# Performance work log

Measured on AMD Instinct MI355X. Metric: run time of the kernel, lower is better.

The kernel has to match this reference:

```python
import jax, jax.numpy as jnp
import numpy as np

N_NODES = 50000
N_EDGES = 400000


def setup_inputs() -> dict:
    key = jax.random.key(0)
    ks = jax.random.split(key, 8)
    d_in, d_hid, d_out = 512, 512, 256
    feats = jax.random.normal(ks[0], (N_NODES, d_in), dtype=jnp.float32)
    src = jax.random.randint(ks[1], (N_EDGES,), 0, N_NODES, dtype=jnp.int32)
    dst = jax.random.randint(ks[2], (N_EDGES,), 0, N_NODES, dtype=jnp.int32)
    # Glorot-ish scaled weights so activations stay O(1)
    W0 = jax.random.normal(ks[3], (d_in, d_hid), dtype=jnp.float32) / np.sqrt(d_in)
    b0 = jnp.zeros((d_hid,), jnp.float32)
    W1 = jax.random.normal(ks[4], (d_hid, d_hid), dtype=jnp.float32) / np.sqrt(d_hid)
    b1 = jnp.zeros((d_hid,), jnp.float32)
    W2 = jax.random.normal(ks[5], (d_hid, d_out), dtype=jnp.float32) / np.sqrt(d_hid)
    b2 = jnp.zeros((d_out,), jnp.float32)
    return {"feats": feats, "src": src, "dst": dst,
            "W0": W0, "b0": b0, "W1": W1, "b1": b1, "W2": W2, "b2": b2}


def _sage_conv_gcn(h, src, dst, W, b, deg):
    # DGL SAGEConv aggregator_type='gcn':
    # h_neigh[v] = (sum_{u->v} h[u] + h[v]) / (in_deg(v) + 1); out = h_neigh @ W + b
    agg = jax.ops.segment_sum(h[src], dst, num_segments=h.shape[0])  # [N, d]
    h_neigh = (agg + h) / (deg[:, None] + 1.0)
    return h_neigh @ W + b


def reference(feats, src, dst, W0, b0, W1, b1, W2, b2):
    N = feats.shape[0]
    deg = jax.ops.segment_sum(jnp.ones((src.shape[0],), feats.dtype), dst,
                              num_segments=N)  # in-degree per node
    h = jax.nn.relu(_sage_conv_gcn(feats, src, dst, W0, b0, deg))  # dropout p=0, norm none
    h = jax.nn.relu(_sage_conv_gcn(h, src, dst, W1, b1, deg))
    h = _sage_conv_gcn(h, src, dst, W2, b2, deg)  # final layer: no activation
    return h
```

## Files before the change

### kernel.cpp

```cpp
#include <hip/hip_runtime.h>
#include <stdint.h>

#define N_NODES 50000
#define N_EDGES 400000
#define MPAD    50048
#define SCAN_B  49

typedef __bf16 bf16x8 __attribute__((ext_vector_type(8)));
typedef float  f32x4  __attribute__((ext_vector_type(4)));
typedef unsigned short ushort_t;
typedef unsigned int   uint_t;

__device__ __forceinline__ ushort_t f2b(float f){
    uint_t x = __float_as_uint(f);
    x += 0x7FFFu + ((x >> 16) & 1u);
    return (ushort_t)(x >> 16);
}
__device__ __forceinline__ float b2f(ushort_t h){
    return __uint_as_float(((uint_t)h) << 16);
}

__global__ void zero_two(int* a, int* b, int n){
    int i = blockIdx.x * blockDim.x + threadIdx.x;
    if (i < n){ a[i] = 0; b[i] = 0; }
}

__global__ void hist_kernel(const int* __restrict__ dst, int* __restrict__ deg, int E){
    int i = blockIdx.x * blockDim.x + threadIdx.x;
    if (i < E) atomicAdd(&deg[dst[i]], 1);
}

__global__ __launch_bounds__(1024) void blk_scan_kernel(
        const int* __restrict__ deg, int* __restrict__ offs,
        int* __restrict__ bsum, int n){
    __shared__ int buf[1024];
    const int t = threadIdx.x, b = blockIdx.x;
    const int i = b * 1024 + t;
    int v = (i < n) ? deg[i] : 0;
    buf[t] = v; __syncthreads();
    for (int off = 1; off < 1024; off <<= 1){
        int x = (t >= off) ? buf[t - off] : 0;
        __syncthreads();
        buf[t] += x;
        __syncthreads();
    }
    if (i < n) offs[i] = buf[t] - v;
    if (t == 1023) bsum[b] = buf[1023];
}

__global__ void bsum_scan_kernel(int* __restrict__ bsum, int nb){
    int t = threadIdx.x;
    int orig = (t < nb) ? bsum[t] : 0;
    int v = orig;
    #pragma unroll
    for (int off = 1; off < 64; off <<= 1){
        int x = __shfl_up(v, off, 64);
        if (t >= off) v += x;
    }
    if (t < nb) bsum[t] = v - orig;
}

__global__ __launch_bounds__(1024) void add_off_kernel(
        int* __restrict__ offs, const int* __restrict__ bsum, int n){
    int i = blockIdx.x * 1024 + threadIdx.x;
    if (i < n) offs[i] += bsum[blockIdx.x];
    if (i == 0) offs[n] = N_EDGES;
}

__global__ void fill_kernel(const int* __restrict__ src, const int* __restrict__ dst,
                            const int* __restrict__ offs, int* __restrict__ cursor,
                            int* __restrict__ nbr, int E){
    int i = blockIdx.x * blockDim.x + threadIdx.x;
    if (i < E){
        int d = dst[i];
        int p = atomicAdd(&cursor[d], 1);
        nbr[offs[d] + p] = src[i];
    }
}

__global__ void wtrans_kernel(const float* __restrict__ W, ushort_t* __restrict__ Wt,
                              int K, int N){
    int i = blockIdx.x * blockDim.x + threadIdx.x;
    if (i < K * N){
        int n = i / K, k = i - n * K;
        Wt[i] = f2b(W[k * N + n]);
    }
}

__device__ __forceinline__ void load16(const void* g, void* l){
    __builtin_amdgcn_global_load_lds((const __attribute__((address_space(1))) void*)g,
                                     (__attribute__((address_space(3))) void*)l, 16, 0, 0);
}

__global__ __launch_bounds__(256, 2) void gemm_bt512(const ushort_t* __restrict__ A,
                                                     const ushort_t* __restrict__ Bt,
                                                     ushort_t* __restrict__ C,
                                                     int K){
    __shared__ ushort_t As[64 * 32];
    __shared__ ushort_t Bs[512 * 32];
    const int tid  = threadIdx.x, lane = tid & 63, wave = tid >> 6;
    const int bm = blockIdx.x;
    const int fr = lane & 15;
    const int fk = (lane >> 4) * 8;
    const int wn = wave * 128;
    f32x4 acc[4][8] = {};

    for (int kt = 0; kt < K; kt += 32){
        __syncthreads();
        {
            int s = tid;
            load16(A + (size_t)(bm * 64 + (s >> 2)) * K + kt + (s & 3) * 8,
                   (char*)As + s * 16);
        }
        #pragma unroll
        for (int i = 0; i < 8; i++){
            int s = tid + i * 256;
            load16(Bt + (size_t)(s >> 2) * K + kt + (s & 3) * 8,
                   (char*)Bs + s * 16);
        }
        __syncthreads();
        bf16x8 af[4], bf[8];
        #pragma unroll
        for (int t = 0; t < 4; t++)
            af[t] = *(const bf16x8*)(const void*)(As + (t * 16 + fr) * 32 + fk);
        #pragma unroll
        for (int t = 0; t < 8; t++)
            bf[t] = *(const bf16x8*)(const void*)(Bs + (wn + t * 16 + fr) * 32 + fk);
        #pragma unroll
        for (int tm = 0; tm < 4; tm++)
            #pragma unroll
            for (int tn = 0; tn < 8; tn++)
                acc[tm][tn] = __builtin_amdgcn_mfma_f32_16x16x32_bf16(
                                  af[tm], bf[tn], acc[tm][tn], 0, 0, 0);
    }
    const int r0 = (lane >> 4) * 4, c0 = lane & 15;
    #pragma unroll
    for (int tm = 0; tm < 4; tm++){
        #pragma unroll
        for (int tn = 0; tn < 8; tn++){
            int rbase = bm * 64 + tm * 16 + r0;
            int cidx  = wn + tn * 16 + c0;
            #pragma unroll
            for (int reg = 0; reg < 4; reg++)
                C[(size_t)(rbase + reg) * 512 + cidx] = f2b(acc[tm][tn][reg]);
        }
    }
}

__global__ __launch_bounds__(256, 2) void gemm_a32(const float* __restrict__ A,
                                                   const ushort_t* __restrict__ Bt,
                                                   ushort_t* __restrict__ C,
                                                   int K){
    __shared__ ushort_t As[64 * 32];
    __shared__ ushort_t Bs[512 * 32];
    const int tid  = threadIdx.x, lane = tid & 63, wave = tid >> 6;
    const int bm = blockIdx.x;
    const int fr = lane & 15;
    const int fk = (lane >> 4) * 8;
    const int wn = wave * 128;
    f32x4 acc[4][8] = {};

    for (int kt = 0; kt < K; kt += 32){
        __syncthreads();
        #pragma unroll
        for (int i = 0; i < 8; i++){
            int s = tid + i * 256;
            load16(Bt + (size_t)(s >> 2) * K + kt + (s & 3) * 8,
                   (char*)Bs + s * 16);
        }
        {
            int s = tid;
            int row = bm * 64 + (s >> 2);
            uint4 o = make_uint4(0u, 0u, 0u, 0u);
            if (row < N_NODES){
                const float* p = A + (size_t)row * K + kt + (s & 3) * 8;
                float4 x = *(const float4*)(const void*)p;
                float4 y = *(const float4*)(const void*)(p + 4);
                o.x = (uint_t)f2b(x.x) | ((uint_t)f2b(x.y) << 16);
                o.y = (uint_t)f2b(x.z) | ((uint_t)f2b(x.w) << 16);
                o.z = (uint_t)f2b(y.x) | ((uint_t)f2b(y.y) << 16);
                o.w = (uint_t)f2b(y.z) | ((uint_t)f2b(y.w) << 16);
            }
            *(uint4*)(void*)((char*)As + s * 16) = o;
        }
        __syncthreads();
        bf16x8 af[4], bf[8];
        #pragma unroll
        for (int t = 0; t < 4; t++)
            af[t] = *(const bf16x8*)(const void*)(As + (t * 16 + fr) * 32 + fk);
        #pragma unroll
        for (int t = 0; t < 8; t++)
            bf[t] = *(const bf16x8*)(const void*)(Bs + (wn + t * 16 + fr) * 32 + fk);
        #pragma unroll
        for (int tm = 0; tm < 4; tm++)
            #pragma unroll
            for (int tn = 0; tn < 8; tn++)
                acc[tm][tn] = __builtin_amdgcn_mfma_f32_16x16x32_bf16(
                                  af[tm], bf[tn], acc[tm][tn], 0, 0, 0);
    }
    const int r0 = (lane >> 4) * 4, c0 = lane & 15;
    #pragma unroll
    for (int tm = 0; tm < 4; tm++){
        #pragma unroll
        for (int tn = 0; tn < 8; tn++){
            int rbase = bm * 64 + tm * 16 + r0;
            int cidx  = wn + tn * 16 + c0;
            #pragma unroll
            for (int reg = 0; reg < 4; reg++)
                C[(size_t)(rbase + reg) * 512 + cidx] = f2b(acc[tm][tn][reg]);
        }
    }
}

__global__ __launch_bounds__(256, 2) void gemm_bt(const ushort_t* __restrict__ A,
                                                  const ushort_t* __restrict__ Bt,
                                                  ushort_t* __restrict__ C,
                                                  int N, int K){
    __shared__ ushort_t As[128 * 32];
    __shared__ ushort_t Bs[256 * 32];
    const int tid  = threadIdx.x, lane = tid & 63, wave = tid >> 6;
    const int bm = blockIdx.x, bn = blockIdx.y;
    const int fr = lane & 15;
    const int fk = (lane >> 4) * 8;
    const int wm = (wave >> 1) * 64, wn = (wave & 1) * 128;
    f32x4 acc[4][8] = {};

    for (int kt = 0; kt < K; kt += 32){
        __syncthreads();
        #pragma unroll
        for (int i = 0; i < 2; i++){
            int s = tid + i * 256;
            load16(A + (size_t)(bm * 128 + (s >> 2)) * K + kt + (s & 3) * 8,
                   (char*)As + s * 16);
        }
        #pragma unroll
        for (int i = 0; i < 4; i++){
            int s = tid + i * 256;
            load16(Bt + (size_t)(bn * 256 + (s >> 2)) * K + kt + (s & 3) * 8,
                   (char*)Bs + s * 16);
        }
        __syncthreads();
        bf16x8 af[4], bf[8];
        #pragma unroll
        for (int t = 0; t < 4; t++)
            af[t] = *(const bf16x8*)(const void*)(As + (wm + t * 16 + fr) * 32 + fk);
        #pragma unroll
        for (int t = 0; t < 8; t++)
            bf[t] = *(const bf16x8*)(const void*)(Bs + (wn + t * 16 + fr) * 32 + fk);
        #pragma unroll
        for (int tm = 0; tm < 4; tm++)
            #pragma unroll
            for (int tn = 0; tn < 8; tn++)
                acc[tm][tn] = __builtin_amdgcn_mfma_f32_16x16x32_bf16(
                                  af[tm], bf[tn], acc[tm][tn], 0, 0, 0);
    }
    const int r0 = (lane >> 4) * 4, c0 = lane & 15;
    #pragma unroll
    for (int tm = 0; tm < 4; tm++){
        #pragma unroll
        for (int tn = 0; tn < 8; tn++){
            int rbase = bm * 128 + wm + tm * 16 + r0;
            int cidx  = bn * 256 + wn + tn * 16 + c0;
            #pragma unroll
            for (int reg = 0; reg < 4; reg++)
                C[(size_t)(rbase + reg) * N + cidx] = f2b(acc[tm][tn][reg]);
        }
    }
}

__device__ __forceinline__ void acc8(float* a, uint4 y){
    a[0] += b2f((ushort_t)(y.x & 0xffff)); a[1] += b2f((ushort_t)(y.x >> 16));
    a[2] += b2f((ushort_t)(y.y & 0xffff)); a[3] += b2f((ushort_t)(y.y >> 16));
    a[4] += b2f((ushort_t)(y.z & 0xffff)); a[5] += b2f((ushort_t)(y.z >> 16));
    a[6] += b2f((ushort_t)(y.w & 0xffff)); a[7] += b2f((ushort_t)(y.w >> 16));
}
__device__ __forceinline__ void acc4(float* a, uint2 y){
    a[0] += b2f((ushort_t)(y.x & 0xffff)); a[1] += b2f((ushort_t)(y.x >> 16));
    a[2] += b2f((ushort_t)(y.y & 0xffff)); a[3] += b2f((ushort_t)(y.y >> 16));
}

__global__ __launch_bounds__(512) void agg_relu_kernel(
        const ushort_t* __restrict__ Y, const int* __restrict__ offs,
        const int* __restrict__ nbr, const float* __restrict__ bias,
        ushort_t* __restrict__ H){
    const int lane = threadIdx.x & 63, wv = threadIdx.x >> 6;
    const int v   = blockIdx.x * 4 + (wv >> 1);
    const int off = (wv & 1) * 256 + lane * 4;
    float a[4];
    {   uint2 y = *(const uint2*)(const void*)(Y + (size_t)v * 512 + off);
        a[0] = b2f((ushort_t)(y.x & 0xffff)); a[1] = b2f((ushort_t)(y.x >> 16));
        a[2] = b2f((ushort_t)(y.y & 0xffff)); a[3] = b2f((ushort_t)(y.y >> 16)); }
    const int beg = offs[v], end = offs[v + 1];
    int i = beg;
    for (; i + 8 <= end; i += 8){
        uint2 yy[8];
        #pragma unroll
        for (int j = 0; j < 8; j++){
            int u = nbr[i + j];
            yy[j] = *(const uint2*)(const void*)(Y + (size_t)u * 512 + off);
        }
        #pragma unroll
        for (int j = 0; j < 8; j++) acc4(a, yy[j]);
    }
    for (; i + 4 <= end; i += 4){
        uint2 yy[4];
        #pragma unroll
        for (int j = 0; j < 4; j++){
            int u = nbr[i + j];
            yy[j] = *(const uint2*)(const void*)(Y + (size_t)u * 512 + off);
        }
        #pragma unroll
        for (int j = 0; j < 4; j++) acc4(a, yy[j]);
    }
    for (; i < end; i++){
        int u = nbr[i];
        uint2 y = *(const uint2*)(const void*)(Y + (size_t)u * 512 + off);
        acc4(a, y);
    }
    const float inv = 1.0f / (float)(end - beg + 1);
    float4 bb = ((const float4*)bias)[(wv & 1) * 64 + lane];
    float r[4];
    r[0] = a[0]*inv + bb.x; r[1] = a[1]*inv + bb.y;
    r[2] = a[2]*inv + bb.z; r[3] = a[3]*inv + bb.w;
    #pragma unroll
    for (int j = 0; j < 4; j++) r[j] = r[j] > 0.f ? r[j] : 0.f;
    uint2 o;
    o.x = (uint_t)f2b(r[0]) | ((uint_t)f2b(r[1]) << 16);
    o.y = (uint_t)f2b(r[2]) | ((uint_t)f2b(r[3]) << 16);
    *(uint2*)(void*)(H + (size_t)v * 512 + off) = o;
}

__global__ __launch_bounds__(256) void agg_out_kernel(
        const ushort_t* __restrict__ Y, const int* __restrict__ offs,
        const int* __restrict__ nbr, const float* __restrict__ bias,
        float* __restrict__ out){
    const int lane = threadIdx.x & 63, wave = threadIdx.x >> 6;
    const int v = blockIdx.x * 4 + wave;
    const int off = lane * 4;
    float a[4];
    {   uint2 y = *(const uint2*)(const void*)(Y + (size_t)v * 256 + off);
        a[0] = b2f((ushort_t)(y.x & 0xffff)); a[1] = b2f((ushort_t)(y.x >> 16));
        a[2] = b2f((ushort_t)(y.y & 0xffff)); a[3] = b2f((ushort_t)(y.y >> 16)); }
    const int beg = offs[v], end = offs[v + 1];
    int i = beg;
    for (; i + 8 <= end; i += 8){
        uint2 yy[8];
        #pragma unroll
        for (int j = 0; j < 8; j++){
            int u = nbr[i + j];
            yy[j] = *(const uint2*)(const void*)(Y + (size_t)u * 256 + off);
        }
        #pragma unroll
        for (int j = 0; j < 8; j++) acc4(a, yy[j]);
    }
    for (; i + 4 <= end; i += 4){
        uint2 yy[4];
        #pragma unroll
        for (int j = 0; j < 4; j++){
            int u = nbr[i + j];
            yy[j] = *(const uint2*)(const void*)(Y + (size_t)u * 256 + off);
        }
        #pragma unroll
        for (int j = 0; j < 4; j++) acc4(a, yy[j]);
    }
    for (; i < end; i++){
        int u = nbr[i];
        uint2 y = *(const uint2*)(const void*)(Y + (size_t)u * 256 + off);
        acc4(a, y);
    }
    const float inv = 1.0f / (float)(end - beg + 1);
    float4 bb = ((const float4*)bias)[lane];
    float4 r;
    r.x = a[0]*inv + bb.x; r.y = a[1]*inv + bb.y;
    r.z = a[2]*inv + bb.z; r.w = a[3]*inv + bb.w;
    ((float4*)out)[v * 64 + lane] = r;
}

extern "C" void kernel_launch(void* const* d_in, const int* in_sizes, int n_in,
                              void* d_out, int out_size, void* d_ws, size_t ws_size,
                              hipStream_t stream) {
    const float* feats = (const float*)d_in[0];
    const int*   src   = (const int*)  d_in[1];
    const int*   dst   = (const int*)  d_in[2];
    const float* W0    = (const float*)d_in[3];
    const float* b0    = (const float*)d_in[4];
    const float* W1    = (const float*)d_in[5];
    const float* b1    = (const float*)d_in[6];
    const float* W2    = (const float*)d_in[7];
    const float* b2    = (const float*)d_in[8];
    float* out = (float*)d_out;

    char* w = (char*)d_ws;
    ushort_t* Abuf = (ushort_t*)w;  w += (size_t)MPAD * 512 * 2;
    ushort_t* Ybuf = (ushort_t*)w;  w += (size_t)MPAD * 512 * 2;
    ushort_t* W0t  = (ushort_t*)w;  w += 512 * 512 * 2;
    ushort_t* W1t  = (ushort_t*)w;  w += 512 * 512 * 2;
    ushort_t* W2t  = (ushort_t*)w;  w += 256 * 512 * 2;
    int* deg    = (int*)w;          w += 50048 * 4;
    int* offs   = (int*)w;          w += 50056 * 4;
    int* cursor = (int*)w;          w += 50048 * 4;
    int* nbr    = (int*)w;          w += (size_t)N_EDGES * 4;
    int* bsum   = (int*)w;          w += 64 * 4;

    zero_two<<<(N_NODES + 255) / 256, 256, 0, stream>>>(deg, cursor, N_NODES);
    hist_kernel<<<(N_EDGES + 255) / 256, 256, 0, stream>>>(dst, deg, N_EDGES);
    blk_scan_kernel<<<SCAN_B, 1024, 0, stream>>>(deg, offs, bsum, N_NODES);
    bsum_scan_kernel<<<1, 64, 0, stream>>>(bsum, SCAN_B);
    add_off_kernel<<<SCAN_B, 1024, 0, stream>>>(offs, bsum, N_NODES);
    fill_kernel<<<(N_EDGES + 255) / 256, 256, 0, stream>>>(src, dst, offs, cursor, nbr, N_EDGES);

    wtrans_kernel<<<(512 * 512 + 255) / 256, 256, 0, stream>>>(W0, W0t, 512, 512);
    wtrans_kernel<<<(512 * 512 + 255) / 256, 256, 0, stream>>>(W1, W1t, 512, 512);
    wtrans_kernel<<<(512 * 256 + 255) / 256, 256, 0, stream>>>(W2, W2t, 512, 256);

    gemm_a32<<<MPAD / 64, 256, 0, stream>>>(feats, W0t, Ybuf, 512);
    agg_relu_kernel<<<N_NODES / 4, 512, 0, stream>>>(Ybuf, offs, nbr, b0, Abuf);
    gemm_bt512<<<MPAD / 64, 256, 0, stream>>>(Abuf, W1t, Ybuf, 512);
    agg_relu_kernel<<<N_NODES / 4, 512, 0, stream>>>(Ybuf, offs, nbr, b1, Abuf);
    dim3 g2(MPAD / 128, 1);
    gemm_bt<<<g2, 256, 0, stream>>>(Abuf, W2t, Ybuf, 256, 512);
    agg_out_kernel<<<N_NODES / 4, 256, 0, stream>>>(Ybuf, offs, nbr, b2, out);
}
```

Baseline: 519.1 us.

## Replace GEMMs with unified 128x128 tile kernel using XOR-swizzled LDS and K=64 steps

The three per-layer GEMM kernels are replaced by 128x128-tile kernels that use a 2D grid over rows and output columns. Each tile advances K in steps of 64 and stores data in LDS with an XOR swizzle to avoid bank conflicts on fragment reads. The fp32-input variant now issues all of its global loads before converting to bf16. Launch bounds allow more blocks per CU, which is meant to raise occupancy and reduce LDS conflicts, but each block now reloads A once per column tile.

```diff
diff --git a/kernel.cpp b/kernel.cpp
--- a/kernel.cpp
+++ b/kernel.cpp
@@ -92,119 +92,141 @@
                                      (__attribute__((address_space(3))) void*)l, 16, 0, 0);
 }
 
-__global__ __launch_bounds__(256, 2) void gemm_bt512(const ushort_t* __restrict__ A,
+__global__ __launch_bounds__(256, 4) void gemm128_bt(const ushort_t* __restrict__ A,
                                                      const ushort_t* __restrict__ Bt,
                                                      ushort_t* __restrict__ C,
-                                                     int K){
-    __shared__ ushort_t As[64 * 32];
-    __shared__ ushort_t Bs[512 * 32];
+                                                     int N, int K){
+    __shared__ ushort_t As[128 * 64];
+    __shared__ ushort_t Bs[128 * 64];
     const int tid  = threadIdx.x, lane = tid & 63, wave = tid >> 6;
-    const int bm = blockIdx.x;
+    const int bm = blockIdx.x, bn = blockIdx.y;
     const int fr = lane & 15;
-    const int fk = (lane >> 4) * 8;
-    const int wn = wave * 128;
-    f32x4 acc[4][8] = {};
-
-    for (int kt = 0; kt < K; kt += 32){
-        __syncthreads();
-        {
-            int s = tid;
-            load16(A + (size_t)(bm * 64 + (s >> 2)) * K + kt + (s & 3) * 8,
+    const int wm = (wave >> 1) * 64, wn = (wave & 1) * 64;
+    f32x4 acc[4][4] = {};
+
+    for (int kt = 0; kt < K; kt += 64){
+        __syncthreads();
+        #pragma unroll
+        for (int i = 0; i < 4; i++){
+            int s = tid + i * 256;
+            int row = s >> 3, p = s & 7, c = p ^ (row & 7);
+            load16(A + (size_t)(bm * 128 + row) * K + kt + c * 8,
                    (char*)As + s * 16);
         }
         #pragma unroll
-        for (int i = 0; i < 8; i++){
-            int s = tid + i * 256;
-            load16(Bt + (size_t)(s >> 2) * K + kt + (s & 3) * 8,
+        for (int i = 0; i < 4; i++){
+            int s = tid + i * 256;
+            int row = s >> 3, p = s & 7, c = p ^ (row & 7);
+            load16(Bt + (size_t)(bn * 128 + row) * K + kt + c * 8,
                    (char*)Bs + s * 16);
         }
         __syncthreads();
-        bf16x8 af[4], bf[8];
-        #pragma unroll
-        for (int t = 0; t < 4; t++)
-            af[t] = *(const bf16x8*)(const void*)(As + (t * 16 + fr) * 32 + fk);
-        #pragma unroll
-        for (int t = 0; t < 8; t++)
-            bf[t] = *(const bf16x8*)(const void*)(Bs + (wn + t * 16 + fr) * 32 + fk);
-        #pragma unroll
-        for (int tm = 0; tm < 4; tm++)
-            #pragma unroll
-            for (int tn = 0; tn < 8; tn++)
-                acc[tm][tn] = __builtin_amdgcn_mfma_f32_16x16x32_bf16(
-                                  af[tm], bf[tn], acc[tm][tn], 0, 0, 0);
+        #pragma unroll
+        for (int ks = 0; ks < 2; ks++){
+            const int c = (lane >> 4) + ks * 4;
+            const int cx = c ^ (fr & 7);
+            bf16x8 af[4], bf[4];
+            #pragma unroll
+            for (int t = 0; t < 4; t++)
+                af[t] = *(const bf16x8*)(const void*)(As + (wm + t * 16 + fr) * 64 + cx * 8);
+            #pragma unroll
+            for (int t = 0; t < 4; t++)
+                bf[t] = *(const bf16x8*)(const void*)(Bs + (wn + t * 16 + fr) * 64 + cx * 8);
+            #pragma unroll
+            for (int tm = 0; tm < 4; tm++)
+                #pragma unroll
+                for (int tn = 0; tn < 4; tn++)
+                    acc[tm][tn] = __builtin_amdgcn_mfma_f32_16x16x32_bf16(
+                                      af[tm], bf[tn], acc[tm][tn], 0, 0, 0);
+        }
     }
     const int r0 = (lane >> 4) * 4, c0 = lane & 15;
     #pragma unroll
     for (int tm = 0; tm < 4; tm++){
         #pragma unroll
-        for (int tn = 0; tn < 8; tn++){
-            int rbase = bm * 64 + tm * 16 + r0;
-            int cidx  = wn + tn * 16 + c0;
+        for (int tn = 0; tn < 4; tn++){
+            int rbase = bm * 128 + wm + tm * 16 + r0;
+            int cidx  = bn * 128 + wn + tn * 16 + c0;
             #pragma unroll
             for (int reg = 0; reg < 4; reg++)
-                C[(size_t)(rbase + reg) * 512 + cidx] = f2b(acc[tm][tn][reg]);
-        }
-    }
-}
-
-__global__ __launch_bounds__(256, 2) void gemm_a32(const float* __restrict__ A,
-                                                   const ushort_t* __restrict__ Bt,
-                                                   ushort_t* __restrict__ C,
-                                                   int K){
-    __shared__ ushort_t As[64 * 32];
-    __shared__ ushort_t Bs[512 * 32];
+                C[(size_t)(rbase + reg) * N + cidx] = f2b(acc[tm][tn][reg]);
+        }
+    }
+}
+
+__global__ __launch_bounds__(256, 3) void gemm128_a32(const float* __restrict__ A,
+                                                      const ushort_t* __restrict__ Bt,
+                                                      ushort_t* __restrict__ C,
+                                                      int K){
+    __shared__ ushort_t As[128 * 64];
+    __shared__ ushort_t Bs[128 * 64];
     const int tid  = threadIdx.x, lane = tid & 63, wave = tid >> 6;
-    const int bm = blockIdx.x;
+    const int bm = blockIdx.x, bn = blockIdx.y;
     const int fr = lane & 15;
-    const int fk = (lane >> 4) * 8;
-    const int wn = wave * 128;
-    f32x4 acc[4][8] = {};
-
-    for (int kt = 0; kt < K; kt += 32){
-        __syncthreads();
-        #pragma unroll
-        for (int i = 0; i < 8; i++){
-            int s = tid + i * 256;
-            load16(Bt + (size_t)(s >> 2) * K + kt + (s & 3) * 8,
+    const int wm = (wave >> 1) * 64, wn = (wave & 1) * 64;
+    f32x4 acc[4][4] = {};
+
+    for (int kt = 0; kt < K; kt += 64){
+        __syncthreads();
+        float4 x[4], y[4];
+        #pragma unroll
+        for (int i = 0; i < 4; i++){
+            int s = tid + i * 256;
+            int row = s >> 3, p = s & 7, c = p ^ (row & 7);
+            int grow = bm * 128 + row;
+            if (grow < N_NODES){
+                const float* pp = A + (size_t)grow * K + kt + c * 8;
+                x[i] = *(const float4*)(const void*)pp;
+                y[i] = *(const float4*)(const void*)(pp + 4);
+            } else {
+                x[i] = make_float4(0.f, 0.f, 0.f, 0.f);
+                y[i] = make_float4(0.f, 0.f, 0.f, 0.f);
+            }
+        }
+        #pragma unroll
+        for (int i = 0; i < 4; i++){
+            int s = tid + i * 256;
+            int row = s >> 3, p = s & 7, c = p ^ (row & 7);
+            load16(Bt + (size_t)(bn * 128 + row) * K + kt + c * 8,
                    (char*)Bs + s * 16);
         }
-        {
-            int s = tid;
-            int row = bm * 64 + (s >> 2);
-            uint4 o = make_uint4(0u, 0u, 0u, 0u);
-            if (row < N_NODES){
-                const float* p = A + (size_t)row * K + kt + (s & 3) * 8;
-                float4 x = *(const float4*)(const void*)p;
-                float4 y = *(const float4*)(const void*)(p + 4);
-                o.x = (uint_t)f2b(x.x) | ((uint_t)f2b(x.y) << 16);
-                o.y = (uint_t)f2b(x.z) | ((uint_t)f2b(x.w) << 16);
-                o.z = (uint_t)f2b(y.x) | ((uint_t)f2b(y.y) << 16);
-                o.w = (uint_t)f2b(y.z) | ((uint_t)f2b(y.w) << 16);
-            }
+        #pragma unroll
+        for (int i = 0; i < 4; i++){
+            int s = tid + i * 256;
+            uint4 o;
+            o.x = (uint_t)f2b(x[i].x) | ((uint_t)f2b(x[i].y) << 16);
+            o.y = (uint_t)f2b(x[i].z) | ((uint_t)f2b(x[i].w) << 16);
+            o.z = (uint_t)f2b(y[i].x) | ((uint_t)f2b(y[i].y) << 16);
+            o.w = (uint_t)f2b(y[i].z) | ((uint_t)f2b(y[i].w) << 16);
             *(uint4*)(void*)((char*)As + s * 16) = o;
         }
         __syncthreads();
-        bf16x8 af[4], bf[8];
-        #pragma unroll
-        for (int t = 0; t < 4; t++)
-            af[t] = *(const bf16x8*)(const void*)(As + (t * 16 + fr) * 32 + fk);
-        #pragma unroll
-        for (int t = 0; t < 8; t++)
-            bf[t] = *(const bf16x8*)(const void*)(Bs + (wn + t * 16 + fr) * 32 + fk);
-        #pragma unroll
-        for (int tm = 0; tm < 4; tm++)
-            #pragma unroll
-            for (int tn = 0; tn < 8; tn++)
-                acc[tm][tn] = __builtin_amdgcn_mfma_f32_16x16x32_bf16(
-                                  af[tm], bf[tn], acc[tm][tn], 0, 0, 0);
+        #pragma unroll
+        for (int ks = 0; ks < 2; ks++){
+            const int c = (lane >> 4) + ks * 4;
+            const int cx = c ^ (fr & 7);
+            bf16x8 af[4], bf[4];
+            #pragma unroll
+            for (int t = 0; t < 4; t++)
+                af[t] = *(const bf16x8*)(const void*)(As + (wm + t * 16 + fr) * 64 + cx * 8);
+            #pragma unroll
+            for (int t = 0; t < 4; t++)
+                bf[t] = *(const bf16x8*)(const void*)(Bs + (wn + t * 16 + fr) * 64 + cx * 8);
+            #pragma unroll
+            for (int tm = 0; tm < 4; tm++)
+                #pragma unroll
+                for (int tn = 0; tn < 4; tn++)
+                    acc[tm][tn] = __builtin_amdgcn_mfma_f32_16x16x32_bf16(
+                                      af[tm], bf[tn], acc[tm][tn], 0, 0, 0);
+        }
     }
     const int r0 = (lane >> 4) * 4, c0 = lane & 15;
     #pragma unroll
     for (int tm = 0; tm < 4; tm++){
         #pragma unroll
-        for (int tn = 0; tn < 8; tn++){
-            int rbase = bm * 64 + tm * 16 + r0;
-            int cidx  = wn + tn * 16 + c0;
+        for (int tn = 0; tn < 4; tn++){
+            int rbase = bm * 128 + wm + tm * 16 + r0;
+            int cidx  = bn * 128 + wn + tn * 16 + c0;
             #pragma unroll
             for (int reg = 0; reg < 4; reg++)
                 C[(size_t)(rbase + reg) * 512 + cidx] = f2b(acc[tm][tn][reg]);
@@ -212,68 +234,6 @@
     }
 }
 
-__global__ __launch_bounds__(256, 2) void gemm_bt(const ushort_t* __restrict__ A,
-                                                  const ushort_t* __restrict__ Bt,
-                                                  ushort_t* __restrict__ C,
-                                                  int N, int K){
-    __shared__ ushort_t As[128 * 32];
-    __shared__ ushort_t Bs[256 * 32];
-    const int tid  = threadIdx.x, lane = tid & 63, wave = tid >> 6;
-    const int bm = blockIdx.x, bn = blockIdx.y;
-    const int fr = lane & 15;
-    const int fk = (lane >> 4) * 8;
-    const int wm = (wave >> 1) * 64, wn = (wave & 1) * 128;
-    f32x4 acc[4][8] = {};
-
-    for (int kt = 0; kt < K; kt += 32){
-        __syncthreads();
-        #pragma unroll
-        for (int i = 0; i < 2; i++){
-            int s = tid + i * 256;
-            load16(A + (size_t)(bm * 128 + (s >> 2)) * K + kt + (s & 3) * 8,
-                   (char*)As + s * 16);
-        }
-        #pragma unroll
-        for (int i = 0; i < 4; i++){
-            int s = tid + i * 256;
-            load16(Bt + (size_t)(bn * 256 + (s >> 2)) * K + kt + (s & 3) * 8,
-                   (char*)Bs + s * 16);
-        }
-        __syncthreads();
-        bf16x8 af[4], bf[8];
-        #pragma unroll
-        for (int t = 0; t < 4; t++)
-            af[t] = *(const bf16x8*)(const void*)(As + (wm + t * 16 + fr) * 32 + fk);
-        #pragma unroll
-        for (int t = 0; t < 8; t++)
-            bf[t] = *(const bf16x8*)(const void*)(Bs + (wn + t * 16 + fr) * 32 + fk);
-        #pragma unroll
-        for (int tm = 0; tm < 4; tm++)
-            #pragma unroll
-            for (int tn = 0; tn < 8; tn++)
-                acc[tm][tn] = __builtin_amdgcn_mfma_f32_16x16x32_bf16(
-                                  af[tm], bf[tn], acc[tm][tn], 0, 0, 0);
-    }
-    const int r0 = (lane >> 4) * 4, c0 = lane & 15;
-    #pragma unroll
-    for (int tm = 0; tm < 4; tm++){
-        #pragma unroll
-        for (int tn = 0; tn < 8; tn++){
-            int rbase = bm * 128 + wm + tm * 16 + r0;
-            int cidx  = bn * 256 + wn + tn * 16 + c0;
-            #pragma unroll
-            for (int reg = 0; reg < 4; reg++)
-                C[(size_t)(rbase + reg) * N + cidx] = f2b(acc[tm][tn][reg]);
-        }
-    }
-}
-
-__device__ __forceinline__ void acc8(float* a, uint4 y){
-    a[0] += b2f((ushort_t)(y.x & 0xffff)); a[1] += b2f((ushort_t)(y.x >> 16));
-    a[2] += b2f((ushort_t)(y.y & 0xffff)); a[3] += b2f((ushort_t)(y.y >> 16));
-    a[4] += b2f((ushort_t)(y.z & 0xffff)); a[5] += b2f((ushort_t)(y.z >> 16));
-    a[6] += b2f((ushort_t)(y.w & 0xffff)); a[7] += b2f((ushort_t)(y.w >> 16));
-}
 __device__ __forceinline__ void acc4(float* a, uint2 y){
     a[0] += b2f((ushort_t)(y.x & 0xffff)); a[1] += b2f((ushort_t)(y.x >> 16));
     a[2] += b2f((ushort_t)(y.y & 0xffff)); a[3] += b2f((ushort_t)(y.y >> 16));
@@ -413,11 +373,13 @@
     wtrans_kernel<<<(512 * 512 + 255) / 256, 256, 0, stream>>>(W1, W1t, 512, 512);
     wtrans_kernel<<<(512 * 256 + 255) / 256, 256, 0, stream>>>(W2, W2t, 512, 256);
 
-    gemm_a32<<<MPAD / 64, 256, 0, stream>>>(feats, W0t, Ybuf, 512);
+    dim3 g01(MPAD / 128, 512 / 128);
+    dim3 g2 (MPAD / 128, 256 / 128);
+
+    gemm128_a32<<<g01, 256, 0, stream>>>(feats, W0t, Ybuf, 512);
     agg_relu_kernel<<<N_NODES / 4, 512, 0, stream>>>(Ybuf, offs, nbr, b0, Abuf);
-    gemm_bt512<<<MPAD / 64, 256, 0, stream>>>(Abuf, W1t, Ybuf, 512);
+    gemm128_bt<<<g01, 256, 0, stream>>>(Abuf, W1t, Ybuf, 512, 512);
     agg_relu_kernel<<<N_NODES / 4, 512, 0, stream>>>(Ybuf, offs, nbr, b1, Abuf);
-    dim3 g2(MPAD / 128, 1);
-    gemm_bt<<<g2, 256, 0, stream>>>(Abuf, W2t, Ybuf, 256, 512);
+    gemm128_bt<<<g2, 256, 0, stream>>>(Abuf, W2t, Ybuf, 256, 512);
     agg_out_kernel<<<N_NODES / 4, 256, 0, stream>>>(Ybuf, offs, nbr, b2, out);
 }
```

New measurement: 512.3 us. About the same (-1.3%).
